# Optimization experiments

Measured on AMD Instinct MI355X. Metric: run time of the kernel, lower is better.

The kernel has to match this reference:

```python
import jax, jax.numpy as jnp
import numpy as np

NEG_INF = jnp.float32(-1e30)
HASH_PRIME = jnp.int32(1000003)
BLANK_INDEX = 0
BEAM_WIDTH = 32
TOP_PATHS = 1


def _beam_search_single(logp, length):
    """CTC prefix beam search for one utterance.
    logp: [T, C] log-probabilities. length: scalar int32.
    Returns (neg_log_prob [P], lengths [P], labels [P, T]).
    """
    T, C = logp.shape
    W = BEAM_WIDTH
    classes = jnp.arange(C, dtype=jnp.int32)
    tpos = jnp.arange(T, dtype=jnp.int32)
    N = W + W * C  # stay candidates + extend candidates

    seqs0 = jnp.zeros((W, T), jnp.int32)
    lens0 = jnp.zeros((W,), jnp.int32)
    hashes0 = jnp.arange(W, dtype=jnp.int32)  # distinct -> no spurious merging
    pb0 = jnp.full((W,), NEG_INF, jnp.float32).at[0].set(0.0)  # empty prefix, ends-in-blank
    pnb0 = jnp.full((W,), NEG_INF, jnp.float32)

    def step(state, inp):
        seqs, lens, hashes, pb, pnb = state
        lp, t = inp  # lp: [C]
        last = jnp.where(lens > 0, seqs[jnp.arange(W), jnp.maximum(lens - 1, 0)], -1)
        lp_last = jnp.where(last >= 0, lp[jnp.maximum(last, 0)], NEG_INF)
        ptot = jnp.logaddexp(pb, pnb)
        # --- stay candidates (same prefix): blank emission + repeated last label
        stay_pb = ptot + lp[BLANK_INDEX]
        stay_pnb = pnb + lp_last
        # --- extend candidates (W, C): prefix + c, c != blank
        ext_pnb = jnp.where(classes[None, :] == last[:, None],
                            pb[:, None] + lp[None, :],      # repeat label needs blank gap
                            ptot[:, None] + lp[None, :])
        ext_pnb = jnp.where(classes[None, :] == BLANK_INDEX, NEG_INF, ext_pnb)
        ext_pb = jnp.full((W, C), NEG_INF, jnp.float32)
        ext_hash = hashes[:, None] * HASH_PRIME + (classes[None, :] + 1)
        cand_pb = jnp.concatenate([stay_pb, ext_pb.reshape(-1)])
        cand_pnb = jnp.concatenate([stay_pnb, ext_pnb.reshape(-1)])
        cand_hash = jnp.concatenate([hashes, ext_hash.reshape(-1)])
        # --- merge candidates sharing the same prefix (by rolling hash)
        order = jnp.argsort(cand_hash)
        h_s = cand_hash[order]
        pb_s, pnb_s = cand_pb[order], cand_pnb[order]
        new_seg = jnp.concatenate([jnp.ones((1,), jnp.int32),
                                   (h_s[1:] != h_s[:-1]).astype(jnp.int32)])
        seg_id = jnp.cumsum(new_seg) - 1

        def seg_lse(x):
            m = jax.ops.segment_max(x, seg_id, num_segments=N)
            s = jax.ops.segment_sum(jnp.exp(x - m[seg_id]), seg_id, num_segments=N)
            return m + jnp.log(s)

        pb_m = seg_lse(pb_s)[seg_id]
        pnb_m = seg_lse(pnb_s)[seg_id]
        first = new_seg == 1
        pb_s = jnp.where(first, pb_m, NEG_INF)
        pnb_s = jnp.where(first, pnb_m, NEG_INF)
        tot = jnp.logaddexp(pb_s, pnb_s)
        # --- beam pruning
        _, top_idx = jax.lax.top_k(tot, W)
        sel = order[top_idx]  # indices into flat candidate list
        is_ext = sel >= W
        parent = jnp.where(is_ext, (sel - W) // C, sel)
        cls = jnp.where(is_ext, (sel - W) % C, 0).astype(jnp.int32)
        new_pb = pb_s[top_idx]
        new_pnb = pnb_s[top_idx]
        new_hash = cand_hash[sel]
        p_seqs = seqs[parent]
        p_lens = lens[parent]
        new_seqs = jnp.where(is_ext[:, None] & (tpos[None, :] == p_lens[:, None]),
                             cls[:, None], p_seqs)
        new_lens = p_lens + is_ext.astype(jnp.int32)
        # only advance while t < data_length
        active = t < length
        seqs = jnp.where(active, new_seqs, seqs)
        lens = jnp.where(active, new_lens, lens)
        hashes = jnp.where(active, new_hash, hashes)
        pb = jnp.where(active, new_pb, pb)
        pnb = jnp.where(active, new_pnb, pnb)
        return (seqs, lens, hashes, pb, pnb), None

    (seqs, lens, hashes, pb, pnb), _ = jax.lax.scan(
        step, (seqs0, lens0, hashes0, pb0, pnb0), (logp, tpos))
    tot = jnp.logaddexp(pb, pnb)
    top_tot, top_i = jax.lax.top_k(tot, TOP_PATHS)
    return -top_tot, lens[top_i], seqs[top_i]


def setup_inputs() -> dict:
    key = jax.random.key(0)
    k1, k2 = jax.random.split(key)
    data = jax.random.normal(k1, (512, 64, 128), jnp.float32)
    data = jax.nn.log_softmax(data, axis=-1)  # layer expects log probs (from_logits=False)
    data_length = jax.random.randint(k2, (64,), 1, 513, dtype=jnp.int32)
    return {"data": data, "data_length": data_length}


def reference(data, data_length):
    # data: [max_time, batch, num_classes] log probs -> [batch, T, C]
    logp = jnp.transpose(data, (1, 0, 2))
    probs, lengths, predicted = jax.vmap(_beam_search_single)(logp, data_length)
    # top_paths == 1 path of _select_most_likely_path: plain reshape
    B = predicted.shape[0]
    T = predicted.shape[2]
    best = predicted.reshape(B, T)
    lens = lengths.reshape(B)
    # _mask_out_junk_values: fill positions >= length with blank_index
    mask = jnp.arange(T, dtype=lens.dtype)[None, :] < lens[:, None]
    return jnp.where(mask, best, jnp.int32(BLANK_INDEX))
```

## Files before the change

### kernel.cpp

```cpp
#include <hip/hip_runtime.h>
#include <stdint.h>

#define T_MAX 512
#define BATCH 64
#define NCLS  128
#define BEAM  32
#define TBL   6144
#define NEGF  (-1e30f)
#define EMPTYK ((int)0x80000000)
#define HPRIME 1000003u
#define SCAP  256

__device__ __forceinline__ float lae(float a, float b) {
  float mx = fmaxf(a, b);
  return mx + log1pf(expf(-fabsf(a - b)));
}
__device__ __forceinline__ unsigned encf(float x) {
  unsigned b = __float_as_uint(x);
  return (b & 0x80000000u) ? ~b : (b | 0x80000000u);
}
__device__ __forceinline__ float decf(unsigned u) {
  unsigned b = (u & 0x80000000u) ? (u ^ 0x80000000u) : ~u;
  return __uint_as_float(b);
}

__device__ __forceinline__ int tbl_insert(int* key, int h) {
  unsigned x = (unsigned)h * 2654435761u;
  x ^= x >> 16;
  int j = (int)(((unsigned long long)x * (unsigned long long)TBL) >> 32);
  for (;;) {
    int cur = key[j];
    if (cur == EMPTYK) cur = atomicCAS(&key[j], EMPTYK, h);
    if (cur == EMPTYK || cur == h) return j;
    ++j; if (j == TBL) j = 0;
  }
}

__device__ __forceinline__ unsigned long long shflx64(unsigned long long v, int m) {
  unsigned lo = (unsigned)__shfl_xor((int)(unsigned)v, m, 64);
  unsigned hi = (unsigned)__shfl_xor((int)(unsigned)(v >> 32), m, 64);
  return ((unsigned long long)hi << 32) | lo;
}

__global__ __launch_bounds__(512, 1)
void ctc_beam_kernel(const float* __restrict__ data,
                     const int* __restrict__ dlen,
                     int* __restrict__ out) {
  __shared__ int       tkey[TBL];
  __shared__ unsigned  tmax[TBL];
  __shared__ unsigned  tsum[TBL];
  __shared__ unsigned  tmin[TBL];
  __shared__ unsigned short bp[T_MAX * BEAM];
  __shared__ float lpbuf[2][NCLS];
  __shared__ int   bhash[2][BEAM];
  __shared__ float bpb[2][BEAM], bpnb[2][BEAM];
  __shared__ int   blen[2][BEAM], blast[2][BEAM];
  __shared__ float sptot[BEAM], s_pb[BEAM], s_pnb[BEAM], s_pnbm[BEAM];
  __shared__ int   stay_slot[BEAM];
  __shared__ unsigned char mergeTo[BEAM * NCLS];
  __shared__ int mergeCnt[BEAM], mergeFrom[BEAM];
  __shared__ unsigned thsub[64];
  __shared__ int anom, ovf;
  __shared__ int scnt[2];
  __shared__ unsigned thr_s;
  __shared__ unsigned long long skey[SCAP + 16];
  __shared__ unsigned sidx[SCAP];
  __shared__ unsigned long long wkey[8 * BEAM];
  __shared__ unsigned widx[8 * BEAM];
  __shared__ unsigned sel[BEAM];
  __shared__ int seqbuf[T_MAX];
  __shared__ int flen_s;

  const int tid = threadIdx.x;
  const int b = blockIdx.x;
  int L = dlen[b];
  L = L < 0 ? 0 : (L > T_MAX ? T_MAX : L);

  if (tid < BEAM) {
    bhash[0][tid] = tid;
    bpb[0][tid]   = (tid == 0) ? 0.0f : NEGF;
    bpnb[0][tid]  = NEGF;
    blen[0][tid]  = 0;
    blast[0][tid] = -1;
    mergeCnt[tid] = 0;
  }
  {
    unsigned* mtw = (unsigned*)mergeTo;
    for (int m = tid; m < (BEAM * NCLS) / 4; m += 512) mtw[m] = 0xFFFFFFFFu;
  }
  if (tid == 0) { anom = 0; ovf = 0; scnt[0] = 0; scnt[1] = 0; }
  if (tid < NCLS && L > 0) lpbuf[0][tid] = data[(size_t)b * NCLS + tid];
  __syncthreads();

  int cb = 0;
  for (int t = 0; t < L; ++t) {
    const int par = t & 1;
    const bool haspre = (tid >= 256) && (tid < 256 + NCLS) && (t + 1 < L);
    float pre = 0.0f;
    if (haspre) pre = data[((size_t)(t + 1) * BATCH + b) * NCLS + (tid - 256)];
    float* lpc = lpbuf[par];

    if (tid < BEAM) {
      const float pbv = bpb[cb][tid], pnbv = bpnb[cb][tid];
      const float pt = lae(pbv, pnbv);
      sptot[tid] = pt;
      s_pb[tid]  = pt + lpc[0];
      const int lsti = blast[cb][tid];
      s_pnb[tid] = pnbv + ((lsti >= 0) ? lpc[lsti] : NEGF);
      thsub[32 + tid] = 0u;
    }
    for (int k = tid; k < BEAM * BEAM; k += 512) {
      const int j = k >> 5, i2 = k & 31;
      const unsigned hj = (unsigned)bhash[cb][j];
      const unsigned hip = (unsigned)bhash[cb][i2] * HPRIME;
      const unsigned c = hj - hip - 1u;
      if (c < (unsigned)NCLS) {
        atomicAdd(&mergeCnt[j], 1);
        mergeFrom[j] = (i2 << 8) | (int)c;
        mergeTo[i2 * NCLS + (int)c] = (unsigned char)j;
      }
      if (j < i2) {
        const unsigned d = ((unsigned)bhash[cb][j] - (unsigned)bhash[cb][i2]) * HPRIME;
        if (d + 127u <= 254u) anom = 1;
      }
    }
    __syncthreads();

    const int i  = tid >> 4;
    const int c0 = (tid & 15) << 3;
    unsigned long long k8[8];
    {
      const float pbi = bpb[cb][i];
      const float pti = sptot[i];
      const int   lsti = blast[cb][i];
      const unsigned hb = (unsigned)bhash[cb][i] * HPRIME;
      const float4 l0 = ((const float4*)(lpc + c0))[0];
      const float4 l1 = ((const float4*)(lpc + c0))[1];
      const float lv[8] = {l0.x, l0.y, l0.z, l0.w, l1.x, l1.y, l1.z, l1.w};
      const unsigned m0 = ((const unsigned*)&mergeTo[i * NCLS + c0])[0];
      const unsigned m1 = ((const unsigned*)&mergeTo[i * NCLS + c0])[1];
      unsigned pbest = 0u;
      #pragma unroll
      for (int k = 0; k < 8; ++k) {
        const int c = c0 + k;
        const unsigned mb = ((k < 4 ? (m0 >> (8 * k)) : (m1 >> (8 * (k - 4)))) & 0xFFu);
        const float x = (c == 0) ? NEGF : (((c == lsti) ? pbi : pti) + lv[k]);
        const float tot = fmaxf(x, NEGF);
        const unsigned h = hb + (unsigned)(c + 1);
        unsigned long long key =
            ((unsigned long long)encf(tot) << 32) |
            (unsigned long long)(0xFFFFFFFFu - (h ^ 0x80000000u));
        if (mb != 0xFFu || c == 0) key = 0ull;
        k8[k] = key;
        const unsigned e32 = (unsigned)(key >> 32);
        pbest = pbest > e32 ? pbest : e32;
      }
      atomicMax(&thsub[32 + i], pbest);
    }
    if (tid < BEAM) {
      const int j = tid;
      if (mergeCnt[j] > 1) anom = 1;
      float pnbm;
      if (mergeCnt[j] == 1) {
        const int mf = mergeFrom[j];
        const int mi = mf >> 8, mc = mf & 255;
        const float e = (mc == 0) ? NEGF
            : (((mc == blast[cb][mi]) ? bpb[cb][mi] : sptot[mi]) + lpc[mc]);
        const float a = s_pnb[j];
        const float m = fmaxf(a, e);
        const float s = expf(a - m) + expf(e - m);
        pnbm = m + logf(s);
      } else {
        pnbm = s_pnb[j];
      }
      s_pnbm[j] = pnbm;
      thsub[j] = encf(lae(s_pb[j], pnbm));
    }
    if (tid == 511) scnt[par ^ 1] = 0;
    __syncthreads();

    const bool an = (anom != 0);
    bool dorare = an;
    if (!an) {
      if (tid < 64) {
        const unsigned vq = thsub[tid];
        int rank = 0;
        #pragma unroll
        for (int p = 0; p < 64; ++p) {
          const unsigned vp = thsub[p];
          rank += (vp > vq || (vp == vq && p < tid)) ? 1 : 0;
        }
        if (rank == 31) thr_s = vq;
      } else {
        unsigned* mtw = (unsigned*)mergeTo;
        for (int m = tid - 64; m < (BEAM * NCLS) / 4; m += 448) mtw[m] = 0xFFFFFFFFu;
        if (tid >= 64 && tid < 64 + BEAM) mergeCnt[tid - 64] = 0;
        if (haspre) lpbuf[par ^ 1][tid - 256] = pre;
      }
      __syncthreads();

      const unsigned thr = thr_s;
      int myn = 0;
      #pragma unroll
      for (int k = 0; k < 8; ++k) myn += ((unsigned)(k8[k] >> 32) >= thr) ? 1 : 0;
      const bool stayS = (tid < BEAM) && (thsub[tid] >= thr);
      myn += stayS ? 1 : 0;
      if (myn) {
        int o = atomicAdd(&scnt[par], myn);
        if (o + myn <= SCAP) {
          #pragma unroll
          for (int k = 0; k < 8; ++k) {
            if ((unsigned)(k8[k] >> 32) >= thr) {
              skey[o] = k8[k];
              sidx[o] = (unsigned)(BEAM + i * NCLS + (c0 + k));
              ++o;
            }
          }
          if (stayS) {
            skey[o] = ((unsigned long long)thsub[tid] << 32) |
                      (unsigned long long)(0xFFFFFFFFu - ((unsigned)bhash[cb][tid] ^ 0x80000000u));
            sidx[o] = (unsigned)tid;
          }
        } else ovf = 1;
      }
      __syncthreads();
      dorare = (ovf != 0);
    }

    if (!dorare) {
      const int scr = scnt[par];
      if (tid < scr) {
        const unsigned long long kq = skey[tid];
        int rank = 0;
        for (int p0 = 0; p0 < scr; p0 += 16) {
          #pragma unroll
          for (int pp = 0; pp < 16; ++pp) {
            const unsigned long long kp = skey[p0 + pp];
            rank += ((p0 + pp) < scr && kp > kq) ? 1 : 0;
          }
        }
        if (rank < BEAM) {
          const int j = rank;
          const unsigned s = sidx[tid];
          int nh, p, cls, ex; float npb, npnb;
          if (s < BEAM) {
            p = (int)s; cls = 0; ex = 0;
            nh = bhash[cb][p];
            npb = s_pb[p];
            npnb = s_pnbm[p];
          } else {
            const unsigned q = s - BEAM;
            p = (int)(q >> 7); cls = (int)(q & 127); ex = 1;
            nh = (int)((unsigned)bhash[cb][p] * HPRIME + (unsigned)(cls + 1));
            npb = NEGF;
            npnb = (cls == 0) ? NEGF
                 : (((cls == blast[cb][p]) ? bpb[cb][p] : sptot[p]) + lpc[cls]);
          }
          const int plen = blen[cb][p], plast = blast[cb][p];
          const int nb = cb ^ 1;
          bhash[nb][j] = nh; bpb[nb][j] = npb; bpnb[nb][j] = npnb;
          blen[nb][j]  = plen + ex;
          blast[nb][j] = ex ? cls : plast;
          bp[t * BEAM + j] = (unsigned short)(p | (cls << 5) | (ex << 12));
        }
      }
      __syncthreads();
    } else {
      for (int m = tid; m < TBL; m += 512) {
        tkey[m] = EMPTYK; tmax[m] = 0u; tsum[m] = 0u; tmin[m] = 0xFFFFFFFFu;
      }
      __syncthreads();

      int eslot[8]; float ex_[8];
      {
        const float pbi = bpb[cb][i];
        const float pti = sptot[i];
        const int   lsti = blast[cb][i];
        const unsigned hb = (unsigned)bhash[cb][i] * HPRIME;
        #pragma unroll
        for (int k = 0; k < 8; ++k) {
          const int c = c0 + k;
          int h = (int)(hb + (unsigned)(c + 1));
          if (h == EMPTYK) h = (int)0x80000001u;
          const float x = (c == 0) ? NEGF : (((c == lsti) ? pbi : pti) + lpc[c]);
          const int s = tbl_insert(tkey, h);
          atomicMax(&tmax[s], encf(x));
          atomicMin(&tmin[s], (unsigned)(BEAM + i * NCLS + c));
          eslot[k] = s; ex_[k] = x;
        }
      }
      if (tid < BEAM) {
        const int s = tbl_insert(tkey, bhash[cb][tid]);
        atomicMax(&tmax[s], encf(s_pnb[tid]));
        atomicMin(&tmin[s], (unsigned)tid);
        stay_slot[tid] = s;
      }
      __syncthreads();

      #pragma unroll
      for (int k = 0; k < 8; ++k) {
        const int s = eslot[k];
        atomicAdd((float*)&tsum[s], expf(ex_[k] - decf(tmax[s])));
      }
      if (tid < BEAM) {
        const int s = stay_slot[tid];
        atomicAdd((float*)&tsum[s], expf(s_pnb[tid] - decf(tmax[s])));
      }
      __syncthreads();

      for (int m = tid; m < TBL; m += 512) {
        if (tkey[m] != EMPTYK) {
          const float mm = decf(tmax[m]);
          const float ss = __uint_as_float(tsum[m]);
          const float pnbm = mm + logf(ss);
          tmax[m] = __float_as_uint(pnbm);
          tsum[m] = encf(lae(NEGF, pnbm));
        }
      }
      __syncthreads();
      if (tid < BEAM) {
        const int s = stay_slot[tid];
        tsum[s] = encf(lae(s_pb[tid], __uint_as_float(tmax[s])));
      }
      __syncthreads();

      {
        const int wv = tid >> 6, ln = tid & 63;
        const int base = wv * (TBL / 8) + ln * (TBL / 512);
        unsigned long long kk2[TBL / 512];
        #pragma unroll
        for (int m = 0; m < TBL / 512; ++m) {
          const int idx = base + m;
          if (tkey[idx] != EMPTYK) {
            const unsigned hh = (unsigned)tkey[idx] ^ 0x80000000u;
            kk2[m] = ((unsigned long long)tsum[idx] << 32) |
                     (unsigned long long)(0xFFFFFFFFu - hh);
          } else kk2[m] = 0ull;
        }
        unsigned cons = 0;
        for (int it = 0; it < BEAM; ++it) {
          unsigned long long best = 0ull; int bi = -1;
          #pragma unroll
          for (int m = 0; m < TBL / 512; ++m)
            if (!((cons >> m) & 1u) && kk2[m] > best) { best = kk2[m]; bi = m; }
          unsigned long long wm = best;
          #pragma unroll
          for (int off = 32; off > 0; off >>= 1) {
            const unsigned long long o = shflx64(wm, off);
            if (o > wm) wm = o;
          }
          const unsigned long long ball = __ballot(best == wm && wm != 0ull);
          const int winner = ball ? (__ffsll((long long)ball) - 1) : -1;
          if (ln == winner) {
            cons |= 1u << bi;
            wkey[wv * BEAM + it] = wm;
            widx[wv * BEAM + it] = (unsigned)(base + bi);
          } else if (winner < 0 && ln == 0) {
            wkey[wv * BEAM + it] = 0ull;
            widx[wv * BEAM + it] = 0xFFFFFFFFu;
          }
        }
      }
      __syncthreads();
      if (tid < 64) {
        unsigned long long kk2[4]; unsigned ii[4];
        #pragma unroll
        for (int m = 0; m < 4; ++m) { kk2[m] = wkey[tid * 4 + m]; ii[m] = widx[tid * 4 + m]; }
        unsigned cons = 0;
        for (int it = 0; it < BEAM; ++it) {
          unsigned long long best = 0ull; int bi = -1;
          #pragma unroll
          for (int m = 0; m < 4; ++m)
            if (!((cons >> m) & 1u) && kk2[m] > best) { best = kk2[m]; bi = m; }
          unsigned long long wm = best;
          #pragma unroll
          for (int off = 32; off > 0; off >>= 1) {
            const unsigned long long o = shflx64(wm, off);
            if (o > wm) wm = o;
          }
          const unsigned long long ball = __ballot(best == wm && wm != 0ull);
          const int winner = ball ? (__ffsll((long long)ball) - 1) : -1;
          if (tid == winner) { cons |= 1u << bi; sel[it] = ii[bi]; }
          else if (winner < 0 && tid == 0) sel[it] = 0xFFFFFFFFu;
        }
      }
      __syncthreads();

      if (tid < BEAM) {
        const int j = tid;
        const unsigned s = sel[j];
        int nh, p, cls, ex; float npb, npnb;
        if (s != 0xFFFFFFFFu) {
          nh = tkey[s];
          npnb = __uint_as_float(tmax[s]);
          npb = NEGF;
          #pragma unroll
          for (int q = 0; q < BEAM; ++q)
            if (stay_slot[q] == (int)s) npb = s_pb[q];
          const unsigned mi = tmin[s];
          ex  = (mi >= BEAM) ? 1 : 0;
          p   = ex ? (int)((mi - BEAM) >> 7) : (int)mi;
          cls = ex ? (int)((mi - BEAM) & 127) : 0;
          p &= 31;
        } else {
          nh = 0x7F000000 + j; npb = NEGF; npnb = NEGF; p = j; cls = 0; ex = 0;
        }
        const int plen = blen[cb][p], plast = blast[cb][p];
        const int nb = cb ^ 1;
        bhash[nb][j] = nh; bpb[nb][j] = npb; bpnb[nb][j] = npnb;
        blen[nb][j]  = plen + ex;
        blast[nb][j] = ex ? cls : plast;
        bp[t * BEAM + j] = (unsigned short)(p | (cls << 5) | (ex << 12));
      }
      {
        unsigned* mtw = (unsigned*)mergeTo;
        for (int m = tid; m < (BEAM * NCLS) / 4; m += 512) mtw[m] = 0xFFFFFFFFu;
      }
      if (tid >= 64 && tid < 64 + BEAM) mergeCnt[tid - 64] = 0;
      if (tid == 511) { anom = 0; ovf = 0; }
      if (haspre) lpbuf[par ^ 1][tid - 256] = pre;
      __syncthreads();
    }
    cb ^= 1;
  }

  if (tid == 0) {
    float bt = -3.4e38f; int bj = 0;
    for (int j = 0; j < BEAM; ++j) {
      const float tt = lae(bpb[cb][j], bpnb[cb][j]);
      if (tt > bt) { bt = tt; bj = j; }
    }
    int cur = bj;
    int pos = blen[cb][bj];
    flen_s = pos;
    for (int tt = L - 1; tt >= 0; --tt) {
      const unsigned short e = bp[tt * BEAM + cur];
      const int p = e & 31, cl = (e >> 5) & 127, ex = (e >> 12) & 1;
      if (ex) { --pos; if (pos >= 0) seqbuf[pos] = cl; }
      cur = p;
    }
  }
  __syncthreads();
  const int fl = flen_s;
  for (int k = tid; k < T_MAX; k += 512) {
    out[(size_t)b * T_MAX + k] = (k < fl) ? seqbuf[k] : 0;
  }
}

extern "C" void kernel_launch(void* const* d_in, const int* in_sizes, int n_in,
                              void* d_out, int out_size, void* d_ws, size_t ws_size,
                              hipStream_t stream) {
  const float* data = (const float*)d_in[0];
  const int*   dlen = (const int*)d_in[1];
  int* out = (int*)d_out;
  (void)in_sizes; (void)n_in; (void)out_size; (void)d_ws; (void)ws_size;
  hipLaunchKernelGGL(ctc_beam_kernel, dim3(BATCH), dim3(512), 0, stream,
                     data, dlen, out);
}
```

Baseline: 2.629 ms.

## Shrink beam block to a single wavefront using wave-level ballot and scan

Cuts the block from 512 threads to 64 so that each utterance runs on one wavefront. Shared atomics and flags (anomaly, overflow, candidate counter, threshold) become wave intrinsics: __any, ballot/shfl for the threshold, and a shfl_up prefix scan for compaction. Each lane now handles 64 classes held in registers. The aim is to remove the block-wide barriers and shared-memory atomics on the serial per-timestep path. In exchange each thread does 8x more work, which raises register pressure, and the rare hash-table path loses parallelism and now recomputes its inserts.

```diff
diff --git a/kernel.cpp b/kernel.cpp
--- a/kernel.cpp
+++ b/kernel.cpp
@@ -16,12 +16,15 @@
   return mx + log1pf(expf(-fabsf(a - b)));
 }
 __device__ __forceinline__ unsigned encf(float x) {
-  unsigned b = __float_as_uint(x);
-  return (b & 0x80000000u) ? ~b : (b | 0x80000000u);
+  unsigned v = __float_as_uint(x);
+  return (v & 0x80000000u) ? ~v : (v | 0x80000000u);
 }
 __device__ __forceinline__ float decf(unsigned u) {
-  unsigned b = (u & 0x80000000u) ? (u ^ 0x80000000u) : ~u;
-  return __uint_as_float(b);
+  unsigned v = (u & 0x80000000u) ? (u ^ 0x80000000u) : ~u;
+  return __uint_as_float(v);
+}
+__device__ __forceinline__ unsigned lowkey(unsigned h) {
+  return 0xFFFFFFFFu - (h ^ 0x80000000u);
 }
 
 __device__ __forceinline__ int tbl_insert(int* key, int h) {
@@ -42,7 +45,7 @@
   return ((unsigned long long)hi << 32) | lo;
 }
 
-__global__ __launch_bounds__(512, 1)
+__global__ __launch_bounds__(64, 1)
 void ctc_beam_kernel(const float* __restrict__ data,
                      const int* __restrict__ dlen,
                      int* __restrict__ out) {
@@ -51,7 +54,7 @@
   __shared__ unsigned  tsum[TBL];
   __shared__ unsigned  tmin[TBL];
   __shared__ unsigned short bp[T_MAX * BEAM];
-  __shared__ float lpbuf[2][NCLS];
+  __shared__ __align__(16) float lpbuf[2][NCLS];
   __shared__ int   bhash[2][BEAM];
   __shared__ float bpb[2][BEAM], bpnb[2][BEAM];
   __shared__ int   blen[2][BEAM], blast[2][BEAM];
@@ -60,13 +63,8 @@
   __shared__ unsigned char mergeTo[BEAM * NCLS];
   __shared__ int mergeCnt[BEAM], mergeFrom[BEAM];
   __shared__ unsigned thsub[64];
-  __shared__ int anom, ovf;
-  __shared__ int scnt[2];
-  __shared__ unsigned thr_s;
   __shared__ unsigned long long skey[SCAP + 16];
   __shared__ unsigned sidx[SCAP];
-  __shared__ unsigned long long wkey[8 * BEAM];
-  __shared__ unsigned widx[8 * BEAM];
   __shared__ unsigned sel[BEAM];
   __shared__ int seqbuf[T_MAX];
   __shared__ int flen_s;
@@ -86,19 +84,23 @@
   }
   {
     unsigned* mtw = (unsigned*)mergeTo;
-    for (int m = tid; m < (BEAM * NCLS) / 4; m += 512) mtw[m] = 0xFFFFFFFFu;
-  }
-  if (tid == 0) { anom = 0; ovf = 0; scnt[0] = 0; scnt[1] = 0; }
-  if (tid < NCLS && L > 0) lpbuf[0][tid] = data[(size_t)b * NCLS + tid];
+    for (int m = tid; m < (BEAM * NCLS) / 4; m += 64) mtw[m] = 0xFFFFFFFFu;
+  }
+  if (L > 0) {
+    lpbuf[0][tid * 2 + 0] = data[(size_t)b * NCLS + tid * 2 + 0];
+    lpbuf[0][tid * 2 + 1] = data[(size_t)b * NCLS + tid * 2 + 1];
+  }
   __syncthreads();
 
   int cb = 0;
   for (int t = 0; t < L; ++t) {
     const int par = t & 1;
-    const bool haspre = (tid >= 256) && (tid < 256 + NCLS) && (t + 1 < L);
-    float pre = 0.0f;
-    if (haspre) pre = data[((size_t)(t + 1) * BATCH + b) * NCLS + (tid - 256)];
+    const bool haspre = (t + 1 < L);
+    float2 pf = make_float2(0.f, 0.f);
+    if (haspre)
+      pf = *(const float2*)(data + ((size_t)(t + 1) * BATCH + b) * NCLS + tid * 2);
     float* lpc = lpbuf[par];
+    int anomr = 0;
 
     if (tid < BEAM) {
       const float pbv = bpb[cb][tid], pnbv = bpnb[cb][tid];
@@ -109,7 +111,7 @@
       s_pnb[tid] = pnbv + ((lsti >= 0) ? lpc[lsti] : NEGF);
       thsub[32 + tid] = 0u;
     }
-    for (int k = tid; k < BEAM * BEAM; k += 512) {
+    for (int k = tid; k < BEAM * BEAM; k += 64) {
       const int j = k >> 5, i2 = k & 31;
       const unsigned hj = (unsigned)bhash[cb][j];
       const unsigned hip = (unsigned)bhash[cb][i2] * HPRIME;
@@ -120,46 +122,46 @@
         mergeTo[i2 * NCLS + (int)c] = (unsigned char)j;
       }
       if (j < i2) {
-        const unsigned d = ((unsigned)bhash[cb][j] - (unsigned)bhash[cb][i2]) * HPRIME;
-        if (d + 127u <= 254u) anom = 1;
+        const unsigned d = (hj - (unsigned)bhash[cb][i2]) * HPRIME;
+        if (d + 127u <= 254u) anomr = 1;
       }
     }
     __syncthreads();
 
-    const int i  = tid >> 4;
-    const int c0 = (tid & 15) << 3;
-    unsigned long long k8[8];
+    const int i  = tid >> 1;
+    const int c0 = (tid & 1) << 6;
+    unsigned e32[64];
+    unsigned hbr;
     {
       const float pbi = bpb[cb][i];
       const float pti = sptot[i];
       const int   lsti = blast[cb][i];
-      const unsigned hb = (unsigned)bhash[cb][i] * HPRIME;
-      const float4 l0 = ((const float4*)(lpc + c0))[0];
-      const float4 l1 = ((const float4*)(lpc + c0))[1];
-      const float lv[8] = {l0.x, l0.y, l0.z, l0.w, l1.x, l1.y, l1.z, l1.w};
-      const unsigned m0 = ((const unsigned*)&mergeTo[i * NCLS + c0])[0];
-      const unsigned m1 = ((const unsigned*)&mergeTo[i * NCLS + c0])[1];
+      hbr = (unsigned)bhash[cb][i] * HPRIME;
+      const float4* lp4 = (const float4*)(lpc + c0);
+      const unsigned* mw = (const unsigned*)&mergeTo[i * NCLS + c0];
       unsigned pbest = 0u;
       #pragma unroll
-      for (int k = 0; k < 8; ++k) {
-        const int c = c0 + k;
-        const unsigned mb = ((k < 4 ? (m0 >> (8 * k)) : (m1 >> (8 * (k - 4)))) & 0xFFu);
-        const float x = (c == 0) ? NEGF : (((c == lsti) ? pbi : pti) + lv[k]);
-        const float tot = fmaxf(x, NEGF);
-        const unsigned h = hb + (unsigned)(c + 1);
-        unsigned long long key =
-            ((unsigned long long)encf(tot) << 32) |
-            (unsigned long long)(0xFFFFFFFFu - (h ^ 0x80000000u));
-        if (mb != 0xFFu || c == 0) key = 0ull;
-        k8[k] = key;
-        const unsigned e32 = (unsigned)(key >> 32);
-        pbest = pbest > e32 ? pbest : e32;
+      for (int g = 0; g < 8; ++g) {
+        const float4 l0 = lp4[g * 2], l1 = lp4[g * 2 + 1];
+        const float lv[8] = {l0.x, l0.y, l0.z, l0.w, l1.x, l1.y, l1.z, l1.w};
+        const unsigned m0 = mw[g * 2], m1 = mw[g * 2 + 1];
+        #pragma unroll
+        for (int k = 0; k < 8; ++k) {
+          const int c = c0 + g * 8 + k;
+          const unsigned mb = ((k < 4 ? (m0 >> (8 * k)) : (m1 >> (8 * (k - 4)))) & 0xFFu);
+          const float x = (c == 0) ? NEGF : (((c == lsti) ? pbi : pti) + lv[k]);
+          const float tot = fmaxf(x, NEGF);
+          unsigned enc = encf(tot);
+          if (mb != 0xFFu || c == 0) enc = 0u;
+          e32[g * 8 + k] = enc;
+          pbest = pbest > enc ? pbest : enc;
+        }
       }
       atomicMax(&thsub[32 + i], pbest);
     }
     if (tid < BEAM) {
       const int j = tid;
-      if (mergeCnt[j] > 1) anom = 1;
+      if (mergeCnt[j] > 1) anomr = 1;
       float pnbm;
       if (mergeCnt[j] == 1) {
         const int mf = mergeFrom[j];
@@ -176,117 +178,121 @@
       s_pnbm[j] = pnbm;
       thsub[j] = encf(lae(s_pb[j], pnbm));
     }
-    if (tid == 511) scnt[par ^ 1] = 0;
     __syncthreads();
 
-    const bool an = (anom != 0);
+    const bool an = (__any(anomr) != 0);
     bool dorare = an;
+    int scr = 0;
     if (!an) {
-      if (tid < 64) {
-        const unsigned vq = thsub[tid];
-        int rank = 0;
+      const unsigned vq = thsub[tid];
+      int rank = 0;
+      #pragma unroll
+      for (int p2 = 0; p2 < 64; ++p2) {
+        const unsigned vp = thsub[p2];
+        rank += (vp > vq || (vp == vq && p2 < tid)) ? 1 : 0;
+      }
+      const unsigned long long rb = __ballot(rank == 31);
+      const int rsrc = __ffsll((long long)rb) - 1;
+      const unsigned thr = (unsigned)__shfl((int)vq, rsrc, 64);
+
+      const bool stayS = (tid < BEAM) && (thsub[tid] >= thr);
+      int myn = stayS ? 1 : 0;
+      #pragma unroll
+      for (int k = 0; k < 64; ++k) myn += (e32[k] >= thr) ? 1 : 0;
+      int pfx = myn;
+      #pragma unroll
+      for (int d = 1; d < 64; d <<= 1) {
+        const int o = __shfl_up(pfx, d, 64);
+        if (tid >= d) pfx += o;
+      }
+      scr = __shfl(pfx, 63, 64);
+      if (scr <= SCAP) {
+        int o = pfx - myn;
         #pragma unroll
-        for (int p = 0; p < 64; ++p) {
-          const unsigned vp = thsub[p];
-          rank += (vp > vq || (vp == vq && p < tid)) ? 1 : 0;
-        }
-        if (rank == 31) thr_s = vq;
+        for (int k = 0; k < 64; ++k) {
+          if (e32[k] >= thr) {
+            skey[o] = ((unsigned long long)e32[k] << 32) |
+                      (unsigned long long)lowkey(hbr + (unsigned)(c0 + k + 1));
+            sidx[o] = (unsigned)(BEAM + i * NCLS + (c0 + k));
+            ++o;
+          }
+        }
+        if (stayS) {
+          skey[o] = ((unsigned long long)thsub[tid] << 32) |
+                    (unsigned long long)lowkey((unsigned)bhash[cb][tid]);
+          sidx[o] = (unsigned)tid;
+        }
       } else {
-        unsigned* mtw = (unsigned*)mergeTo;
-        for (int m = tid - 64; m < (BEAM * NCLS) / 4; m += 448) mtw[m] = 0xFFFFFFFFu;
-        if (tid >= 64 && tid < 64 + BEAM) mergeCnt[tid - 64] = 0;
-        if (haspre) lpbuf[par ^ 1][tid - 256] = pre;
-      }
-      __syncthreads();
-
-      const unsigned thr = thr_s;
-      int myn = 0;
-      #pragma unroll
-      for (int k = 0; k < 8; ++k) myn += ((unsigned)(k8[k] >> 32) >= thr) ? 1 : 0;
-      const bool stayS = (tid < BEAM) && (thsub[tid] >= thr);
-      myn += stayS ? 1 : 0;
-      if (myn) {
-        int o = atomicAdd(&scnt[par], myn);
-        if (o + myn <= SCAP) {
-          #pragma unroll
-          for (int k = 0; k < 8; ++k) {
-            if ((unsigned)(k8[k] >> 32) >= thr) {
-              skey[o] = k8[k];
-              sidx[o] = (unsigned)(BEAM + i * NCLS + (c0 + k));
-              ++o;
-            }
-          }
-          if (stayS) {
-            skey[o] = ((unsigned long long)thsub[tid] << 32) |
-                      (unsigned long long)(0xFFFFFFFFu - ((unsigned)bhash[cb][tid] ^ 0x80000000u));
-            sidx[o] = (unsigned)tid;
-          }
-        } else ovf = 1;
-      }
-      __syncthreads();
-      dorare = (ovf != 0);
-    }
+        dorare = true;
+      }
+    }
+    __syncthreads();
 
     if (!dorare) {
-      const int scr = scnt[par];
-      if (tid < scr) {
-        const unsigned long long kq = skey[tid];
+      for (int s0 = tid; s0 < scr; s0 += 64) {
+        const unsigned long long kq = skey[s0];
         int rank = 0;
         for (int p0 = 0; p0 < scr; p0 += 16) {
           #pragma unroll
-          for (int pp = 0; pp < 16; ++pp) {
-            const unsigned long long kp = skey[p0 + pp];
-            rank += ((p0 + pp) < scr && kp > kq) ? 1 : 0;
+          for (int pp2 = 0; pp2 < 16; ++pp2) {
+            const unsigned long long kp = skey[p0 + pp2];
+            rank += ((p0 + pp2) < scr && kp > kq) ? 1 : 0;
           }
         }
         if (rank < BEAM) {
           const int j = rank;
-          const unsigned s = sidx[tid];
-          int nh, p, cls, ex; float npb, npnb;
+          const unsigned s = sidx[s0];
+          int nh, pq, cls, ex; float npb, npnb;
           if (s < BEAM) {
-            p = (int)s; cls = 0; ex = 0;
-            nh = bhash[cb][p];
-            npb = s_pb[p];
-            npnb = s_pnbm[p];
+            pq = (int)s; cls = 0; ex = 0;
+            nh = bhash[cb][pq];
+            npb = s_pb[pq];
+            npnb = s_pnbm[pq];
           } else {
             const unsigned q = s - BEAM;
-            p = (int)(q >> 7); cls = (int)(q & 127); ex = 1;
-            nh = (int)((unsigned)bhash[cb][p] * HPRIME + (unsigned)(cls + 1));
+            pq = (int)(q >> 7); cls = (int)(q & 127); ex = 1;
+            nh = (int)((unsigned)bhash[cb][pq] * HPRIME + (unsigned)(cls + 1));
             npb = NEGF;
             npnb = (cls == 0) ? NEGF
-                 : (((cls == blast[cb][p]) ? bpb[cb][p] : sptot[p]) + lpc[cls]);
+                 : (((cls == blast[cb][pq]) ? bpb[cb][pq] : sptot[pq]) + lpc[cls]);
           }
-          const int plen = blen[cb][p], plast = blast[cb][p];
-          const int nb = cb ^ 1;
-          bhash[nb][j] = nh; bpb[nb][j] = npb; bpnb[nb][j] = npnb;
-          blen[nb][j]  = plen + ex;
-          blast[nb][j] = ex ? cls : plast;
-          bp[t * BEAM + j] = (unsigned short)(p | (cls << 5) | (ex << 12));
-        }
+          const int plen = blen[cb][pq], plast = blast[cb][pq];
+          const int nb2 = cb ^ 1;
+          bhash[nb2][j] = nh; bpb[nb2][j] = npb; bpnb[nb2][j] = npnb;
+          blen[nb2][j]  = plen + ex;
+          blast[nb2][j] = ex ? cls : plast;
+          bp[t * BEAM + j] = (unsigned short)(pq | (cls << 5) | (ex << 12));
+        }
+      }
+      {
+        unsigned* mtw = (unsigned*)mergeTo;
+        #pragma unroll
+        for (int m = 0; m < 16; ++m) mtw[tid + m * 64] = 0xFFFFFFFFu;
+      }
+      if (tid < BEAM) mergeCnt[tid] = 0;
+      if (haspre) {
+        lpbuf[par ^ 1][tid * 2 + 0] = pf.x;
+        lpbuf[par ^ 1][tid * 2 + 1] = pf.y;
       }
       __syncthreads();
     } else {
-      for (int m = tid; m < TBL; m += 512) {
+      for (int m = tid; m < TBL; m += 64) {
         tkey[m] = EMPTYK; tmax[m] = 0u; tsum[m] = 0u; tmin[m] = 0xFFFFFFFFu;
       }
       __syncthreads();
-
-      int eslot[8]; float ex_[8];
       {
         const float pbi = bpb[cb][i];
         const float pti = sptot[i];
         const int   lsti = blast[cb][i];
-        const unsigned hb = (unsigned)bhash[cb][i] * HPRIME;
-        #pragma unroll
-        for (int k = 0; k < 8; ++k) {
+        #pragma unroll 1
+        for (int k = 0; k < 64; ++k) {
           const int c = c0 + k;
-          int h = (int)(hb + (unsigned)(c + 1));
+          int h = (int)(hbr + (unsigned)(c + 1));
           if (h == EMPTYK) h = (int)0x80000001u;
           const float x = (c == 0) ? NEGF : (((c == lsti) ? pbi : pti) + lpc[c]);
           const int s = tbl_insert(tkey, h);
           atomicMax(&tmax[s], encf(x));
           atomicMin(&tmin[s], (unsigned)(BEAM + i * NCLS + c));
-          eslot[k] = s; ex_[k] = x;
         }
       }
       if (tid < BEAM) {
@@ -296,19 +302,26 @@
         stay_slot[tid] = s;
       }
       __syncthreads();
-
-      #pragma unroll
-      for (int k = 0; k < 8; ++k) {
-        const int s = eslot[k];
-        atomicAdd((float*)&tsum[s], expf(ex_[k] - decf(tmax[s])));
+      {
+        const float pbi = bpb[cb][i];
+        const float pti = sptot[i];
+        const int   lsti = blast[cb][i];
+        #pragma unroll 1
+        for (int k = 0; k < 64; ++k) {
+          const int c = c0 + k;
+          int h = (int)(hbr + (unsigned)(c + 1));
+          if (h == EMPTYK) h = (int)0x80000001u;
+          const float x = (c == 0) ? NEGF : (((c == lsti) ? pbi : pti) + lpc[c]);
+          const int s = tbl_insert(tkey, h);
+          atomicAdd((float*)&tsum[s], expf(x - decf(tmax[s])));
+        }
       }
       if (tid < BEAM) {
         const int s = stay_slot[tid];
         atomicAdd((float*)&tsum[s], expf(s_pnb[tid] - decf(tmax[s])));
       }
       __syncthreads();
-
-      for (int m = tid; m < TBL; m += 512) {
+      for (int m = tid; m < TBL; m += 64) {
         if (tkey[m] != EMPTYK) {
           const float mm = decf(tmax[m]);
           const float ss = __uint_as_float(tsum[m]);
@@ -323,102 +336,65 @@
         tsum[s] = encf(lae(s_pb[tid], __uint_as_float(tmax[s])));
       }
       __syncthreads();
-
-      {
-        const int wv = tid >> 6, ln = tid & 63;
-        const int base = wv * (TBL / 8) + ln * (TBL / 512);
-        unsigned long long kk2[TBL / 512];
+      for (int it = 0; it < BEAM; ++it) {
+        unsigned long long bestk = 0ull; int bests = -1;
+        #pragma unroll 4
+        for (int q2 = 0; q2 < TBL / 64; ++q2) {
+          const int idx = tid * (TBL / 64) + q2;
+          if (tkey[idx] != EMPTYK && tsum[idx] != 0u) {
+            const unsigned long long kk =
+                ((unsigned long long)tsum[idx] << 32) |
+                (unsigned long long)lowkey((unsigned)tkey[idx]);
+            if (kk > bestk) { bestk = kk; bests = idx; }
+          }
+        }
+        unsigned long long wm = bestk;
         #pragma unroll
-        for (int m = 0; m < TBL / 512; ++m) {
-          const int idx = base + m;
-          if (tkey[idx] != EMPTYK) {
-            const unsigned hh = (unsigned)tkey[idx] ^ 0x80000000u;
-            kk2[m] = ((unsigned long long)tsum[idx] << 32) |
-                     (unsigned long long)(0xFFFFFFFFu - hh);
-          } else kk2[m] = 0ull;
-        }
-        unsigned cons = 0;
-        for (int it = 0; it < BEAM; ++it) {
-          unsigned long long best = 0ull; int bi = -1;
-          #pragma unroll
-          for (int m = 0; m < TBL / 512; ++m)
-            if (!((cons >> m) & 1u) && kk2[m] > best) { best = kk2[m]; bi = m; }
-          unsigned long long wm = best;
-          #pragma unroll
-          for (int off = 32; off > 0; off >>= 1) {
-            const unsigned long long o = shflx64(wm, off);
-            if (o > wm) wm = o;
-          }
-          const unsigned long long ball = __ballot(best == wm && wm != 0ull);
-          const int winner = ball ? (__ffsll((long long)ball) - 1) : -1;
-          if (ln == winner) {
-            cons |= 1u << bi;
-            wkey[wv * BEAM + it] = wm;
-            widx[wv * BEAM + it] = (unsigned)(base + bi);
-          } else if (winner < 0 && ln == 0) {
-            wkey[wv * BEAM + it] = 0ull;
-            widx[wv * BEAM + it] = 0xFFFFFFFFu;
-          }
-        }
-      }
-      __syncthreads();
-      if (tid < 64) {
-        unsigned long long kk2[4]; unsigned ii[4];
-        #pragma unroll
-        for (int m = 0; m < 4; ++m) { kk2[m] = wkey[tid * 4 + m]; ii[m] = widx[tid * 4 + m]; }
-        unsigned cons = 0;
-        for (int it = 0; it < BEAM; ++it) {
-          unsigned long long best = 0ull; int bi = -1;
-          #pragma unroll
-          for (int m = 0; m < 4; ++m)
-            if (!((cons >> m) & 1u) && kk2[m] > best) { best = kk2[m]; bi = m; }
-          unsigned long long wm = best;
-          #pragma unroll
-          for (int off = 32; off > 0; off >>= 1) {
-            const unsigned long long o = shflx64(wm, off);
-            if (o > wm) wm = o;
-          }
-          const unsigned long long ball = __ballot(best == wm && wm != 0ull);
-          const int winner = ball ? (__ffsll((long long)ball) - 1) : -1;
-          if (tid == winner) { cons |= 1u << bi; sel[it] = ii[bi]; }
-          else if (winner < 0 && tid == 0) sel[it] = 0xFFFFFFFFu;
-        }
-      }
-      __syncthreads();
-
+        for (int off = 32; off > 0; off >>= 1) {
+          const unsigned long long o = shflx64(wm, off);
+          if (o > wm) wm = o;
+        }
+        const unsigned long long ball = __ballot(bestk == wm && wm != 0ull);
+        const int winner = ball ? (__ffsll((long long)ball) - 1) : -1;
+        if (tid == winner) { sel[it] = (unsigned)bests; tsum[bests] = 0u; }
+        else if (winner < 0 && tid == 0) sel[it] = 0xFFFFFFFFu;
+        __syncthreads();
+      }
       if (tid < BEAM) {
         const int j = tid;
         const unsigned s = sel[j];
-        int nh, p, cls, ex; float npb, npnb;
+        int nh, pq, cls, ex; float npb, npnb;
         if (s != 0xFFFFFFFFu) {
           nh = tkey[s];
           npnb = __uint_as_float(tmax[s]);
           npb = NEGF;
           #pragma unroll
-          for (int q = 0; q < BEAM; ++q)
-            if (stay_slot[q] == (int)s) npb = s_pb[q];
+          for (int q2 = 0; q2 < BEAM; ++q2)
+            if (stay_slot[q2] == (int)s) npb = s_pb[q2];
           const unsigned mi = tmin[s];
           ex  = (mi >= BEAM) ? 1 : 0;
-          p   = ex ? (int)((mi - BEAM) >> 7) : (int)mi;
+          pq  = ex ? (int)((mi - BEAM) >> 7) : (int)mi;
           cls = ex ? (int)((mi - BEAM) & 127) : 0;
-          p &= 31;
+          pq &= 31;
         } else {
-          nh = 0x7F000000 + j; npb = NEGF; npnb = NEGF; p = j; cls = 0; ex = 0;
-        }
-        const int plen = blen[cb][p], plast = blast[cb][p];
-        const int nb = cb ^ 1;
-        bhash[nb][j] = nh; bpb[nb][j] = npb; bpnb[nb][j] = npnb;
-        blen[nb][j]  = plen + ex;
-        blast[nb][j] = ex ? cls : plast;
-        bp[t * BEAM + j] = (unsigned short)(p | (cls << 5) | (ex << 12));
+          nh = 0x7F000000 + j; npb = NEGF; npnb = NEGF; pq = j; cls = 0; ex = 0;
+        }
+        const int plen = blen[cb][pq], plast = blast[cb][pq];
+        const int nb2 = cb ^ 1;
+        bhash[nb2][j] = nh; bpb[nb2][j] = npb; bpnb[nb2][j] = npnb;
+        blen[nb2][j]  = plen + ex;
+        blast[nb2][j] = ex ? cls : plast;
+        bp[t * BEAM + j] = (unsigned short)(pq | (cls << 5) | (ex << 12));
       }
       {
         unsigned* mtw = (unsigned*)mergeTo;
-        for (int m = tid; m < (BEAM * NCLS) / 4; m += 512) mtw[m] = 0xFFFFFFFFu;
-      }
-      if (tid >= 64 && tid < 64 + BEAM) mergeCnt[tid - 64] = 0;
-      if (tid == 511) { anom = 0; ovf = 0; }
-      if (haspre) lpbuf[par ^ 1][tid - 256] = pre;
+        for (int m = tid; m < (BEAM * NCLS) / 4; m += 64) mtw[m] = 0xFFFFFFFFu;
+      }
+      if (tid < BEAM) mergeCnt[tid] = 0;
+      if (haspre) {
+        lpbuf[par ^ 1][tid * 2 + 0] = pf.x;
+        lpbuf[par ^ 1][tid * 2 + 1] = pf.y;
+      }
       __syncthreads();
     }
     cb ^= 1;
@@ -433,17 +409,19 @@
     int cur = bj;
     int pos = blen[cb][bj];
     flen_s = pos;
-    for (int tt = L - 1; tt >= 0; --tt) {
-      const unsigned short e = bp[tt * BEAM + cur];
-      const int p = e & 31, cl = (e >> 5) & 127, ex = (e >> 12) & 1;
-      if (ex) { --pos; if (pos >= 0) seqbuf[pos] = cl; }
-      cur = p;
+    for (int tt2 = L - 1; tt2 >= 0; --tt2) {
+      const unsigned short e = bp[tt2 * BEAM + cur];
+      const int pq = e & 31, cl = (e >> 5) & 127, exq = (e >> 12) & 1;
+      if (exq) { --pos; if (pos >= 0) seqbuf[pos] = cl; }
+      cur = pq;
     }
   }
   __syncthreads();
   const int fl = flen_s;
-  for (int k = tid; k < T_MAX; k += 512) {
-    out[(size_t)b * T_MAX + k] = (k < fl) ? seqbuf[k] : 0;
+  #pragma unroll
+  for (int k = 0; k < 8; ++k) {
+    const int o = tid + k * 64;
+    out[(size_t)b * T_MAX + o] = (o < fl) ? seqbuf[o] : 0;
   }
 }
 
@@ -454,6 +432,6 @@
   const int*   dlen = (const int*)d_in[1];
   int* out = (int*)d_out;
   (void)in_sizes; (void)n_in; (void)out_size; (void)d_ws; (void)ws_size;
-  hipLaunchKernelGGL(ctc_beam_kernel, dim3(BATCH), dim3(512), 0, stream,
+  hipLaunchKernelGGL(ctc_beam_kernel, dim3(BATCH), dim3(64), 0, stream,
                      data, dlen, out);
 }
```

Result: slower. 4.461 ms (+69.7%).
